# Optimization experiments

Measured on AMD Instinct MI355X. Metric: run time of the kernel, lower is better.

Reference implementation:

```python
import jax, jax.numpy as jnp
import numpy as np

WS = 8      # window_size
NH = 4      # num_heads (fixed in module)

def setup_inputs() -> dict:
    key = jax.random.key(0)
    k1, k2, k3 = jax.random.split(key, 3)
    B, C, H, W = 8, 512, 128, 128
    x = jax.random.normal(k1, (B, C, H, W), dtype=jnp.float32)
    # nn.MultiheadAttention parameters (xavier-ish scale)
    w_in = jax.random.normal(k2, (3 * C, C), dtype=jnp.float32) * (1.0 / np.sqrt(C))
    b_in = jnp.zeros((3 * C,), dtype=jnp.float32)
    w_out = jax.random.normal(k3, (C, C), dtype=jnp.float32) * (1.0 / np.sqrt(C))
    b_out = jnp.zeros((C,), dtype=jnp.float32)
    return {"x": x, "w_in": w_in, "b_in": b_in, "w_out": w_out, "b_out": b_out}

def reference(x, w_in, b_in, w_out, b_out):
    B, C, H, W = x.shape
    Hw, Ww = H // WS, W // WS
    hd = C // NH
    # --- window partition: (B,C,H,W) -> (N, L, C), N = B*Hw*Ww, L = WS*WS ---
    xw = x.reshape(B, C, Hw, WS, Ww, WS)
    xw = xw.transpose(0, 2, 4, 1, 3, 5)            # (B,Hw,Ww,C,WS,WS)
    xw = xw.reshape(-1, C, WS * WS)                # (N, C, L)
    xw = xw.transpose(0, 2, 1)                     # (N, L, C)
    N, L, _ = xw.shape
    # --- fused QKV projection (torch MultiheadAttention in_proj) ---
    qkv = jnp.einsum('nlc,ec->nle', xw, w_in) + b_in   # (N, L, 3C)
    q, k, v = jnp.split(qkv, 3, axis=-1)
    q = q.reshape(N, L, NH, hd)
    k = k.reshape(N, L, NH, hd)
    v = v.reshape(N, L, NH, hd)
    scale = 1.0 / np.sqrt(hd)
    scores = jnp.einsum('nqhd,nkhd->nhqk', q, k) * scale   # (N,NH,L,L)
    attn = jax.nn.softmax(scores, axis=-1)
    ctx = jnp.einsum('nhqk,nkhd->nqhd', attn, v).reshape(N, L, C)
    out = jnp.einsum('nlc,oc->nlo', ctx, w_out) + b_out    # (N, L, C)
    # --- window merge: (N,L,C) -> (B,C,H,W) ---
    out = out.transpose(0, 2, 1)                           # (N, C, L)
    out = out.reshape(B, Hw, Ww, C, WS, WS)
    out = out.transpose(0, 3, 1, 4, 2, 5)                  # (B,C,Hw,WS,Ww,WS)
    return out.reshape(B, C, H, W)
```

## Files before the change

kernel.cpp:

```cpp
#include <hip/hip_runtime.h>


typedef __attribute__((ext_vector_type(8))) short s16x8;
typedef __attribute__((ext_vector_type(4))) float f32x4;

#define C_TOT 512
#define HWIMG 128
#define CH_STRIDE (HWIMG * HWIMG)
#define NWIN 2048
#define XW_ELEMS ((size_t)NWIN * 64 * 512)
#define XW_BYTES (XW_ELEMS * 2ull)
#define WIT_ELEMS 786432ull
#define WOT_ELEMS 262144ull
#define WBF_ELEMS 1048576ull
#define WBF_BYTES (WBF_ELEMS * 2ull)
#define CTX_BYTES_FULL (XW_ELEMS * 2ull)

__device__ __forceinline__ unsigned short f2bf(float f) {
  unsigned u = __float_as_uint(f);
  u += 0x7FFFu + ((u >> 16) & 1u);
  return (unsigned short)(u >> 16);
}

__device__ __forceinline__ void gload_lds16(const void* g, void* l) {
  __builtin_amdgcn_global_load_lds(
      (const __attribute__((address_space(1))) unsigned int*)g,
      (__attribute__((address_space(3))) unsigned int*)l, 16, 0, 0);
}

__global__ void conv_w_kernel(const float* __restrict__ w_in,
                              const float* __restrict__ w_out,
                              unsigned short* __restrict__ wbf) {
  int i = blockIdx.x * blockDim.x + threadIdx.x;
  const int NIN = 3 * C_TOT * C_TOT;
  float v = (i < NIN) ? w_in[i] : w_out[i - NIN];
  wbf[i] = f2bf(v);
}

__global__ void conv_wt_kernel(const float* __restrict__ w_in,
                               const float* __restrict__ w_out,
                               unsigned short* __restrict__ wit,
                               unsigned short* __restrict__ wot) {
  int i = blockIdx.x * blockDim.x + threadIdx.x;
  const int NIN = 3 * C_TOT * C_TOT;
  if (i < NIN) {
    const int e = i >> 9, c = i & 511;
    const int t = e >> 9, rem = e & 511;
    const int h = rem >> 7, d = rem & 127;
    const int m = t * 8 + (d >> 4), l = d & 15;
    const int c8 = c >> 3, ec = c & 7;
    wit[(((size_t)(h * 24 + m) * 64 + c8) << 7) + l * 8 + ec] = f2bf(w_in[i]);
  } else {
    const int j = i - NIN;
    const int od = j >> 9, c = j & 511;
    const int m = od >> 4, l = od & 15;
    const int c8 = c >> 3, ec = c & 7;
    wot[(((size_t)m * 64 + c8) << 7) + l * 8 + ec] = f2bf(w_out[j]);
  }
}

__global__ void __launch_bounds__(256)
pack_x_kernel(const float* __restrict__ x, unsigned short* __restrict__ xw) {
  const int n  = blockIdx.x;
  const int bb = n >> 8, hw = (n >> 4) & 15, ww = n & 15;
  const size_t wbase = (size_t)bb * C_TOT * CH_STRIDE
                     + (size_t)(hw * 8) * HWIMG + (size_t)(ww * 8);
  const int tok = threadIdx.x & 63;
  const int q4  = threadIdx.x >> 6;
  const int r = tok >> 3, cc = tok & 7;
  const float* px = x + wbase + (size_t)r * HWIMG + cc;
  unsigned short* pw = xw + (size_t)n * 32768;
#pragma unroll 4
  for (int j = 0; j < 16; ++j) {
    const int o = q4 * 16 + j;
    float v[8];
#pragma unroll
    for (int k = 0; k < 8; ++k) v[k] = px[(size_t)(8 * o + k) * CH_STRIDE];
    s16x8 pk;
#pragma unroll
    for (int k = 0; k < 8; ++k) pk[k] = (short)f2bf(v[k]);
    *(s16x8*)(pw + ((size_t)o * 64 + tok) * 8) = pk;
  }
}

#define BQO 0
#define BKO 16384
#define BVO 32768
#define BXS 49152
#define BPO 49152
#define BLDS 81920

__global__ void __launch_bounds__(512, 4)
qkv_attn_kernel(const unsigned short* __restrict__ xw,
                const float* __restrict__ bin,
                const unsigned short* __restrict__ wit,
                unsigned short* __restrict__ ctx,
                int n0) {
  __shared__ __align__(16) unsigned char sm[BLDS];

  const int tid  = threadIdx.x;
  const int wv   = tid >> 6;
  const int lane = tid & 63;
  const int l15  = lane & 15;
  const int qd   = lane >> 4;
  const int swA  = (l15 & 7) << 4;

  const int h    = blockIdx.x & 3;
  const int nrel = blockIdx.x >> 2;
  const unsigned short* xww = xw + (size_t)(n0 + nrel) * 32768;

  const float SCALE = 0.08838834764831845f;
  const float L2E   = 1.4426950408889634f;

  f32x4 acc[3][4];
#pragma unroll
  for (int a = 0; a < 3; ++a)
#pragma unroll
    for (int b2 = 0; b2 < 4; ++b2) acc[a][b2] = (f32x4){0.f, 0.f, 0.f, 0.f};

  const unsigned short* arow[3];
  int typ[3], d128s[3];
#pragma unroll
  for (int mi = 0; mi < 3; ++mi) {
    const int d0 = 48 * wv + 16 * mi;
    const int t = d0 >> 7;
    const int d128 = d0 & 127;
    typ[mi] = t; d128s[mi] = d128;
    const int m = t * 8 + (d128 >> 4);
    arow[mi] = wit + ((size_t)(h * 24 + m) << 13) + l15 * 8;
  }

#pragma unroll
  for (int p = 0; p < 2; ++p)
    gload_lds16(xww + p * 4096 + tid * 8, &sm[BXS + p * 8192 + (wv << 10)]);
  __syncthreads();

  for (int s = 0; s < 4; ++s) {
    if (s < 3) {
#pragma unroll
      for (int p = 0; p < 2; ++p)
        gload_lds16(xww + (size_t)(s + 1) * 8192 + p * 4096 + tid * 8,
                    &sm[BXS + ((s + 1) & 1) * 16384 + p * 8192 + (wv << 10)]);
    }
    const int cur = BXS + (s & 1) * 16384;
#pragma unroll
    for (int j = 0; j < 4; ++j) {
      const int c8g = 16 * s + 4 * j + qd;
      const int lb = cur + ((4 * j + qd) << 10);
      s16x8 bx[4];
#pragma unroll
      for (int ni = 0; ni < 4; ++ni)
        bx[ni] = *(const s16x8*)(&sm[lb + (16 * ni + l15) * 16]);
#pragma unroll
      for (int mi = 0; mi < 3; ++mi) {
        const s16x8 af = *(const s16x8*)(arow[mi] + ((size_t)c8g << 7));
#pragma unroll
        for (int ni = 0; ni < 4; ++ni)
          acc[mi][ni] = __builtin_amdgcn_mfma_f32_16x16x32_bf16(af, bx[ni], acc[mi][ni], 0, 0, 0);
      }
    }
    __syncthreads();
  }

#pragma unroll
  for (int mi = 0; mi < 3; ++mi) {
    const int t = typ[mi], d128 = d128s[mi];
    const int e0 = t * 512 + h * 128 + d128 + 4 * qd;
    const float bi0 = bin[e0], bi1 = bin[e0 + 1], bi2 = bin[e0 + 2], bi3 = bin[e0 + 3];
#pragma unroll
    for (int ni = 0; ni < 4; ++ni) {
      const int tok = 16 * ni + l15;
      const unsigned short h0 = f2bf(acc[mi][ni][0] + bi0);
      const unsigned short h1 = f2bf(acc[mi][ni][1] + bi1);
      const unsigned short h2 = f2bf(acc[mi][ni][2] + bi2);
      const unsigned short h3 = f2bf(acc[mi][ni][3] + bi3);
      if (t < 2) {
        const unsigned lo = (unsigned)h0 | ((unsigned)h1 << 16);
        const unsigned hi = (unsigned)h2 | ((unsigned)h3 << 16);
        const unsigned long long pk = (unsigned long long)lo | ((unsigned long long)hi << 32);
        const int base = (t == 0) ? BQO : BKO;
        *(unsigned long long*)(&sm[base + tok * 256 + ((2 * (d128 + 4 * qd)) ^ swA)]) = pk;
      } else {
        const int vd = d128 + 4 * qd;
        *(unsigned short*)(&sm[BVO + (vd    ) * 128 + ((2 * tok) ^ (((vd    ) & 7) << 4))]) = h0;
        *(unsigned short*)(&sm[BVO + (vd + 1) * 128 + ((2 * tok) ^ (((vd + 1) & 7) << 4))]) = h1;
        *(unsigned short*)(&sm[BVO + (vd + 2) * 128 + ((2 * tok) ^ (((vd + 2) & 7) << 4))]) = h2;
        *(unsigned short*)(&sm[BVO + (vd + 3) * 128 + ((2 * tok) ^ (((vd + 3) & 7) << 4))]) = h3;
      }
    }
  }
  __syncthreads();

  if (wv < 4) {
    f32x4 s[4];
#pragma unroll
    for (int a = 0; a < 4; ++a) s[a] = (f32x4){0.f, 0.f, 0.f, 0.f};
    const int tqa = 16 * wv + l15;
#pragma unroll
    for (int ks = 0; ks < 4; ++ks) {
      const int c0 = 32 * ks + 8 * qd;
      const s16x8 aq = *(const s16x8*)(&sm[BQO + tqa * 256 + ((2 * c0) ^ swA)]);
#pragma unroll
      for (int ni = 0; ni < 4; ++ni) {
        const int tk = 16 * ni + l15;
        const s16x8 bk = *(const s16x8*)(&sm[BKO + tk * 256 + ((2 * c0) ^ swA)]);
        s[ni] = __builtin_amdgcn_mfma_f32_16x16x32_bf16(aq, bk, s[ni], 0, 0, 0);
      }
    }
    float sv[4][4];
#pragma unroll
    for (int ni = 0; ni < 4; ++ni)
#pragma unroll
      for (int i = 0; i < 4; ++i) sv[ni][i] = s[ni][i] * SCALE;
    float m[4];
#pragma unroll
    for (int i = 0; i < 4; ++i)
      m[i] = fmaxf(fmaxf(sv[0][i], sv[1][i]), fmaxf(sv[2][i], sv[3][i]));
#pragma unroll
    for (int d = 1; d < 16; d <<= 1)
#pragma unroll
      for (int i = 0; i < 4; ++i) m[i] = fmaxf(m[i], __shfl_xor(m[i], d));
    float p[4][4], sum[4] = {0.f, 0.f, 0.f, 0.f};
#pragma unroll
    for (int ni = 0; ni < 4; ++ni)
#pragma unroll
      for (int i = 0; i < 4; ++i) {
        p[ni][i] = exp2f((sv[ni][i] - m[i]) * L2E);
        sum[i] += p[ni][i];
      }
#pragma unroll
    for (int d = 1; d < 16; d <<= 1)
#pragma unroll
      for (int i = 0; i < 4; ++i) sum[i] += __shfl_xor(sum[i], d);
    float rinv[4];
#pragma unroll
    for (int i = 0; i < 4; ++i) rinv[i] = 1.0f / sum[i];
#pragma unroll
    for (int ni = 0; ni < 4; ++ni)
#pragma unroll
      for (int i = 0; i < 4; ++i) {
        const int tqr = 16 * wv + 4 * qd + i;
        const int tk = 16 * ni + l15;
        *(unsigned short*)(&sm[BPO + tqr * 128 + ((2 * tk) ^ ((tqr & 7) << 4))]) =
            f2bf(p[ni][i] * rinv[i]);
      }
  }
  __syncthreads();

  {
    const int mq = wv >> 1;
    const int nb = (wv & 1) * 4;
    f32x4 cacc[4];
#pragma unroll
    for (int a = 0; a < 4; ++a) cacc[a] = (f32x4){0.f, 0.f, 0.f, 0.f};
    const int tqa = 16 * mq + l15;
#pragma unroll
    for (int ks = 0; ks < 2; ++ks) {
      const int c0 = 32 * ks + 8 * qd;
      const s16x8 ap = *(const s16x8*)(&sm[BPO + tqa * 128 + ((2 * c0) ^ swA)]);
#pragma unroll
      for (int j = 0; j < 4; ++j) {
        const int vda = 16 * (nb + j) + l15;
        const s16x8 bv = *(const s16x8*)(&sm[BVO + vda * 128 + ((2 * c0) ^ swA)]);
        cacc[j] = __builtin_amdgcn_mfma_f32_16x16x32_bf16(ap, bv, cacc[j], 0, 0, 0);
      }
    }
    unsigned short* ctxn = ctx + (size_t)nrel * 32768;
#pragma unroll
    for (int j = 0; j < 4; ++j) {
      const int vd = 16 * (nb + j) + l15;
      const int c  = h * 128 + vd;
      const int c8 = c >> 3, e = c & 7;
#pragma unroll
      for (int i = 0; i < 4; ++i) {
        const int tq = 16 * mq + 4 * qd + i;
        ctxn[((size_t)c8 * 64 + tq) * 8 + e] = f2bf(cacc[j][i]);
      }
    }
  }
}

#define OXS 0
#define OLDS 32768

__global__ void __launch_bounds__(512, 4)
outproj_kernel(const unsigned short* __restrict__ ctx,
               const unsigned short* __restrict__ wot,
               const float* __restrict__ bout,
               float* __restrict__ out, int n0) {
  __shared__ __align__(16) unsigned char sm[OLDS];

  const int tid  = threadIdx.x;
  const int wv   = tid >> 6;
  const int lane = tid & 63;
  const int l15  = lane & 15;
  const int qd   = lane >> 4;

  const int nrel = blockIdx.x;
  const int n  = n0 + nrel;
  const int bb = n >> 8, hw = (n >> 4) & 15, ww = n & 15;
  const size_t wbase = (size_t)bb * C_TOT * CH_STRIDE
                     + (size_t)(hw * 8) * HWIMG + (size_t)(ww * 8);
  const unsigned short* ctxn = ctx + (size_t)nrel * 32768;

  f32x4 oacc[4][4];
#pragma unroll
  for (int a = 0; a < 4; ++a)
#pragma unroll
    for (int b2 = 0; b2 < 4; ++b2) oacc[a][b2] = (f32x4){0.f, 0.f, 0.f, 0.f};

  const unsigned short* orow[4];
#pragma unroll
  for (int mo = 0; mo < 4; ++mo)
    orow[mo] = wot + ((size_t)(4 * wv + mo) << 13) + l15 * 8;

#pragma unroll
  for (int p = 0; p < 2; ++p)
    gload_lds16(ctxn + p * 4096 + tid * 8, &sm[OXS + p * 8192 + (wv << 10)]);
  __syncthreads();

  for (int s = 0; s < 4; ++s) {
    if (s < 3) {
#pragma unroll
      for (int p = 0; p < 2; ++p)
        gload_lds16(ctxn + (size_t)(s + 1) * 8192 + p * 4096 + tid * 8,
                    &sm[OXS + ((s + 1) & 1) * 16384 + p * 8192 + (wv << 10)]);
    }
    const int cur = OXS + (s & 1) * 16384;
#pragma unroll
    for (int j = 0; j < 4; ++j) {
      const int c8g = 16 * s + 4 * j + qd;
      const int lb = cur + ((4 * j + qd) << 10);
      s16x8 bc[4];
#pragma unroll
      for (int ni = 0; ni < 4; ++ni)
        bc[ni] = *(const s16x8*)(&sm[lb + (16 * ni + l15) * 16]);
#pragma unroll
      for (int mo = 0; mo < 4; ++mo) {
        const s16x8 af = *(const s16x8*)(orow[mo] + ((size_t)c8g << 7));
#pragma unroll
        for (int ni = 0; ni < 4; ++ni)
          oacc[mo][ni] = __builtin_amdgcn_mfma_f32_16x16x32_bf16(af, bc[ni], oacc[mo][ni], 0, 0, 0);
      }
    }
    __syncthreads();
  }

#pragma unroll
  for (int mo = 0; mo < 4; ++mo) {
    const int od0 = 64 * wv + 16 * mo + 4 * qd;
    float bo[4];
#pragma unroll
    for (int i = 0; i < 4; ++i) bo[i] = bout[od0 + i];
#pragma unroll
    for (int ni = 0; ni < 4; ++ni) {
      const int tok = 16 * ni + l15;
      const int r = tok >> 3, cc = tok & 7;
#pragma unroll
      for (int i = 0; i < 4; ++i) {
        out[wbase + (size_t)(od0 + i) * CH_STRIDE + (size_t)r * HWIMG + cc] =
            oacc[mo][ni][i] + bo[i];
      }
    }
  }
}

#define QO    0
#define KO    16384
#define VO    32768
#define PO    49152
#define CTXO  57344
#define LDSB  73728

__global__ void __launch_bounds__(512, 2)
local_attn_kernel(const unsigned short* __restrict__ xw,
                  const float* __restrict__ bin,
                  const float* __restrict__ bout,
                  const unsigned short* __restrict__ wi,
                  const unsigned short* __restrict__ wo,
                  float* __restrict__ out) {
  __shared__ __align__(16) unsigned char sm[LDSB];
  const int tid  = threadIdx.x;
  const int wv   = tid >> 6;
  const int lane = tid & 63;
  const int l15  = lane & 15;
  const int qd   = lane >> 4;
  const int swA  = (l15 & 7) << 4;
  const int n  = blockIdx.x;
  const int bb = n >> 8;
  const int hw = (n >> 4) & 15;
  const int ww = n & 15;
  const size_t wbase = (size_t)bb * C_TOT * CH_STRIDE
                     + (size_t)(hw * 8) * HWIMG + (size_t)(ww * 8);
  const unsigned short* xww = xw + (size_t)n * 32768;
  f32x4 oacc[4][4];
#pragma unroll
  for (int a = 0; a < 4; ++a)
#pragma unroll
    for (int b2 = 0; b2 < 4; ++b2) oacc[a][b2] = (f32x4){0.f, 0.f, 0.f, 0.f};
  const float SCALE = 0.08838834764831845f;
  const float L2E   = 1.4426950408889634f;
  for (int h = 0; h < 4; ++h) {
    f32x4 acc[3][4];
#pragma unroll
    for (int a = 0; a < 3; ++a)
#pragma unroll
      for (int b2 = 0; b2 < 4; ++b2) acc[a][b2] = (f32x4){0.f, 0.f, 0.f, 0.f};
    const unsigned short* arow[3];
    int typ[3], d128s[3];
#pragma unroll
    for (int mi = 0; mi < 3; ++mi) {
      const int d0 = 48 * wv + 16 * mi;
      const int t = d0 >> 7;
      const int d128 = d0 & 127;
      typ[mi] = t; d128s[mi] = d128;
      arow[mi] = wi + (size_t)(t * 512 + h * 128 + d128 + l15) * 512;
    }
#pragma unroll 4
    for (int ks = 0; ks < 16; ++ks) {
      const int c0 = 32 * ks + 8 * qd;
      const int c8 = c0 >> 3;
      s16x8 bx[4];
#pragma unroll
      for (int ni = 0; ni < 4; ++ni)
        bx[ni] = *(const s16x8*)(xww + ((size_t)c8 * 64 + 16 * ni + l15) * 8);
#pragma unroll
      for (int mi = 0; mi < 3; ++mi) {
        const s16x8 af = *(const s16x8*)(arow[mi] + c0);
#pragma unroll
        for (int ni = 0; ni < 4; ++ni)
          acc[mi][ni] = __builtin_amdgcn_mfma_f32_16x16x32_bf16(af, bx[ni], acc[mi][ni], 0, 0, 0);
      }
    }
#pragma unroll
    for (int mi = 0; mi < 3; ++mi) {
      const int t = typ[mi], d128 = d128s[mi];
      const int e0 = t * 512 + h * 128 + d128 + 4 * qd;
      const float bi0 = bin[e0], bi1 = bin[e0 + 1], bi2 = bin[e0 + 2], bi3 = bin[e0 + 3];
#pragma unroll
      for (int ni = 0; ni < 4; ++ni) {
        const int tok = 16 * ni + l15;
        const unsigned short h0 = f2bf(acc[mi][ni][0] + bi0);
        const unsigned short h1 = f2bf(acc[mi][ni][1] + bi1);
        const unsigned short h2 = f2bf(acc[mi][ni][2] + bi2);
        const unsigned short h3 = f2bf(acc[mi][ni][3] + bi3);
        if (t < 2) {
          const unsigned lo = (unsigned)h0 | ((unsigned)h1 << 16);
          const unsigned hi = (unsigned)h2 | ((unsigned)h3 << 16);
          const unsigned long long pk = (unsigned long long)lo | ((unsigned long long)hi << 32);
          const int base = (t == 0) ? QO : KO;
          *(unsigned long long*)(&sm[base + tok * 256 + ((2 * (d128 + 4 * qd)) ^ swA)]) = pk;
        } else {
          const int vd = d128 + 4 * qd;
          *(unsigned short*)(&sm[VO + (vd    ) * 128 + ((2 * tok) ^ (((vd    ) & 7) << 4))]) = h0;
          *(unsigned short*)(&sm[VO + (vd + 1) * 128 + ((2 * tok) ^ (((vd + 1) & 7) << 4))]) = h1;
          *(unsigned short*)(&sm[VO + (vd + 2) * 128 + ((2 * tok) ^ (((vd + 2) & 7) << 4))]) = h2;
          *(unsigned short*)(&sm[VO + (vd + 3) * 128 + ((2 * tok) ^ (((vd + 3) & 7) << 4))]) = h3;
        }
      }
    }
    __syncthreads();
    if (wv < 4) {
      f32x4 s[4];
#pragma unroll
      for (int a = 0; a < 4; ++a) s[a] = (f32x4){0.f, 0.f, 0.f, 0.f};
      const int tqa = 16 * wv + l15;
#pragma unroll
      for (int ks = 0; ks < 4; ++ks) {
        const int c0 = 32 * ks + 8 * qd;
        const s16x8 aq = *(const s16x8*)(&sm[QO + tqa * 256 + ((2 * c0) ^ swA)]);
#pragma unroll
        for (int ni = 0; ni < 4; ++ni) {
          const int tk = 16 * ni + l15;
          const s16x8 bk = *(const s16x8*)(&sm[KO + tk * 256 + ((2 * c0) ^ swA)]);
          s[ni] = __builtin_amdgcn_mfma_f32_16x16x32_bf16(aq, bk, s[ni], 0, 0, 0);
        }
      }
      float sv[4][4];
#pragma unroll
      for (int ni = 0; ni < 4; ++ni)
#pragma unroll
        for (int i = 0; i < 4; ++i) sv[ni][i] = s[ni][i] * SCALE;
      float m[4];
#pragma unroll
      for (int i = 0; i < 4; ++i)
        m[i] = fmaxf(fmaxf(sv[0][i], sv[1][i]), fmaxf(sv[2][i], sv[3][i]));
#pragma unroll
      for (int d = 1; d < 16; d <<= 1)
#pragma unroll
        for (int i = 0; i < 4; ++i) m[i] = fmaxf(m[i], __shfl_xor(m[i], d));
      float p[4][4], sum[4] = {0.f, 0.f, 0.f, 0.f};
#pragma unroll
      for (int ni = 0; ni < 4; ++ni)
#pragma unroll
        for (int i = 0; i < 4; ++i) {
          p[ni][i] = exp2f((sv[ni][i] - m[i]) * L2E);
          sum[i] += p[ni][i];
        }
#pragma unroll
      for (int d = 1; d < 16; d <<= 1)
#pragma unroll
        for (int i = 0; i < 4; ++i) sum[i] += __shfl_xor(sum[i], d);
      float rinv[4];
#pragma unroll
      for (int i = 0; i < 4; ++i) rinv[i] = 1.0f / sum[i];
#pragma unroll
      for (int ni = 0; ni < 4; ++ni)
#pragma unroll
        for (int i = 0; i < 4; ++i) {
          const int tqr = 16 * wv + 4 * qd + i;
          const int tk = 16 * ni + l15;
          *(unsigned short*)(&sm[PO + tqr * 128 + ((2 * tk) ^ ((tqr & 7) << 4))]) =
              f2bf(p[ni][i] * rinv[i]);
        }
    }
    __syncthreads();
    {
      const int mq = wv >> 1;
      const int nb = (wv & 1) * 4;
      f32x4 cacc[4];
#pragma unroll
      for (int a = 0; a < 4; ++a) cacc[a] = (f32x4){0.f, 0.f, 0.f, 0.f};
      const int tqa = 16 * mq + l15;
#pragma unroll
      for (int ks = 0; ks < 2; ++ks) {
        const int c0 = 32 * ks + 8 * qd;
        const s16x8 ap = *(const s16x8*)(&sm[PO + tqa * 128 + ((2 * c0) ^ swA)]);
#pragma unroll
        for (int j = 0; j < 4; ++j) {
          const int vda = 16 * (nb + j) + l15;
          const s16x8 bv = *(const s16x8*)(&sm[VO + vda * 128 + ((2 * c0) ^ swA)]);
          cacc[j] = __builtin_amdgcn_mfma_f32_16x16x32_bf16(ap, bv, cacc[j], 0, 0, 0);
        }
      }
#pragma unroll
      for (int j = 0; j < 4; ++j)
#pragma unroll
        for (int i = 0; i < 4; ++i) {
          const int tq = 16 * mq + 4 * qd + i;
          const int vd = 16 * (nb + j) + l15;
          *(unsigned short*)(&sm[CTXO + tq * 256 + ((2 * vd) ^ ((tq & 7) << 4))]) =
              f2bf(cacc[j][i]);
        }
    }
    __syncthreads();
    {
#pragma unroll
      for (int ks = 0; ks < 4; ++ks) {
        const int c0 = 32 * ks + 8 * qd;
        s16x8 a2[4];
#pragma unroll
        for (int mo = 0; mo < 4; ++mo) {
          const int od = 64 * wv + 16 * mo + l15;
          a2[mo] = *(const s16x8*)(&wo[(size_t)od * 512 + 128 * h + c0]);
        }
        s16x8 bc[4];
#pragma unroll
        for (int ni = 0; ni < 4; ++ni) {
          const int tok = 16 * ni + l15;
          bc[ni] = *(const s16x8*)(&sm[CTXO + tok * 256 + ((2 * c0) ^ swA)]);
        }
#pragma unroll
        for (int mo = 0; mo < 4; ++mo)
#pragma unroll
          for (int ni = 0; ni < 4; ++ni)
            oacc[mo][ni] = __builtin_amdgcn_mfma_f32_16x16x32_bf16(a2[mo], bc[ni], oacc[mo][ni], 0, 0, 0);
      }
    }
  }
#pragma unroll
  for (int mo = 0; mo < 4; ++mo) {
    const int od0 = 64 * wv + 16 * mo + 4 * qd;
    float bo[4];
#pragma unroll
    for (int i = 0; i < 4; ++i) bo[i] = bout[od0 + i];
#pragma unroll
    for (int ni = 0; ni < 4; ++ni) {
      const int tok = 16 * ni + l15;
      const int r = tok >> 3, cc = tok & 7;
#pragma unroll
      for (int i = 0; i < 4; ++i) {
        out[wbase + (size_t)(od0 + i) * CH_STRIDE + (size_t)r * HWIMG + cc] =
            oacc[mo][ni][i] + bo[i];
      }
    }
  }
}

extern "C" void kernel_launch(void* const* d_in, const int* in_sizes, int n_in,
                              void* d_out, int out_size, void* d_ws, size_t ws_size,
                              hipStream_t stream) {
  const float* x     = (const float*)d_in[0];
  const float* w_in  = (const float*)d_in[1];
  const float* b_in  = (const float*)d_in[2];
  const float* w_out = (const float*)d_in[3];
  const float* b_out = (const float*)d_in[4];
  float* out = (float*)d_out;

  const size_t TIL_BYTES = (WIT_ELEMS + WOT_ELEMS) * 2ull;
  int nc = 0;
  for (int c = 1; c <= 8; c <<= 1) {
    if (ws_size >= XW_BYTES + TIL_BYTES + CTX_BYTES_FULL / (size_t)c) { nc = c; break; }
  }

  if (nc) {
    unsigned short* xwp = (unsigned short*)d_ws;
    unsigned short* wit = xwp + XW_ELEMS;
    unsigned short* wot = wit + WIT_ELEMS;
    unsigned short* ctx = wot + WOT_ELEMS;
    conv_wt_kernel<<<4096, 256, 0, stream>>>(w_in, w_out, wit, wot);
    pack_x_kernel<<<NWIN, 256, 0, stream>>>(x, xwp);
    const int nwc = NWIN / nc;
    for (int k = 0; k < nc; ++k) {
      qkv_attn_kernel<<<nwc * 4, 512, 0, stream>>>(xwp, b_in, wit, ctx, k * nwc);
      outproj_kernel<<<nwc, 512, 0, stream>>>(ctx, wot, b_out, out, k * nwc);
    }
  } else {
    unsigned short* xwp = (unsigned short*)d_ws;
    unsigned short* wbf = xwp + XW_ELEMS;
    conv_w_kernel<<<4096, 256, 0, stream>>>(w_in, w_out, wbf);
    pack_x_kernel<<<NWIN, 256, 0, stream>>>(x, xwp);
    local_attn_kernel<<<NWIN, 512, 0, stream>>>(xwp, b_in, b_out,
                                                wbf, wbf + 786432, out);
  }
}
```

Before: 672.4 us.

## Coalesce pack_x loads with float4 image rows and regroup attention block order

Rewrites the window-packing kernel so each thread reads four consecutive pixels of an image row as a float4 and emits four packed tokens, replacing strided scalar loads with wide coalesced reads of full 128-pixel rows. The old packing kernel is kept as a fallback for the low-workspace path. It also remaps qkv_attn block indices so that eight consecutive blocks cover eight windows for the same head, which changes L2 locality of head weights versus window inputs. The redundant per-lane conversion code adds instruction overhead but should be removed by the compiler.

```diff
diff --git a/kernel.cpp b/kernel.cpp
--- a/kernel.cpp
+++ b/kernel.cpp
@@ -61,25 +61,48 @@
 
 __global__ void __launch_bounds__(256)
 pack_x_kernel(const float* __restrict__ x, unsigned short* __restrict__ xw) {
-  const int n  = blockIdx.x;
-  const int bb = n >> 8, hw = (n >> 4) & 15, ww = n & 15;
-  const size_t wbase = (size_t)bb * C_TOT * CH_STRIDE
-                     + (size_t)(hw * 8) * HWIMG + (size_t)(ww * 8);
-  const int tok = threadIdx.x & 63;
-  const int q4  = threadIdx.x >> 6;
-  const int r = tok >> 3, cc = tok & 7;
-  const float* px = x + wbase + (size_t)r * HWIMG + cc;
+  const int blk = blockIdx.x;
+  const int bb  = blk >> 8;
+  const int hw  = (blk >> 4) & 15;
+  const int og4 = blk & 15;
+  const int t   = threadIdx.x;
+  const int p0  = 4 * t;
+  const int r   = p0 >> 7;
+  const int col0 = p0 & 127;
+  const int n   = bb * 256 + hw * 16 + (col0 >> 3);
+  const int tok0 = r * 8 + (col0 & 7);
+  const float* xs = x + (size_t)bb * C_TOT * CH_STRIDE
+                  + (size_t)hw * 1024 + p0;
   unsigned short* pw = xw + (size_t)n * 32768;
-#pragma unroll 4
-  for (int j = 0; j < 16; ++j) {
-    const int o = q4 * 16 + j;
-    float v[8];
-#pragma unroll
-    for (int k = 0; k < 8; ++k) v[k] = px[(size_t)(8 * o + k) * CH_STRIDE];
-    s16x8 pk;
-#pragma unroll
-    for (int k = 0; k < 8; ++k) pk[k] = (short)f2bf(v[k]);
-    *(s16x8*)(pw + ((size_t)o * 64 + tok) * 8) = pk;
+#pragma unroll
+  for (int jo = 0; jo < 4; ++jo) {
+    const int o = og4 * 4 + jo;
+    float4 f[8];
+#pragma unroll
+    for (int k = 0; k < 8; ++k)
+      f[k] = *(const float4*)(xs + (size_t)(8 * o + k) * CH_STRIDE);
+#pragma unroll
+    for (int i = 0; i < 4; ++i) {
+      s16x8 pk;
+      pk[0] = (short)f2bf(f[0].x); pk[1] = (short)f2bf(f[1].x);
+      pk[2] = (short)f2bf(f[2].x); pk[3] = (short)f2bf(f[3].x);
+      pk[4] = (short)f2bf(f[4].x); pk[5] = (short)f2bf(f[5].x);
+      pk[6] = (short)f2bf(f[6].x); pk[7] = (short)f2bf(f[7].x);
+      if (i == 0) {
+        pk[0]=(short)f2bf(f[0].x); pk[1]=(short)f2bf(f[1].x); pk[2]=(short)f2bf(f[2].x); pk[3]=(short)f2bf(f[3].x);
+        pk[4]=(short)f2bf(f[4].x); pk[5]=(short)f2bf(f[5].x); pk[6]=(short)f2bf(f[6].x); pk[7]=(short)f2bf(f[7].x);
+      } else if (i == 1) {
+        pk[0]=(short)f2bf(f[0].y); pk[1]=(short)f2bf(f[1].y); pk[2]=(short)f2bf(f[2].y); pk[3]=(short)f2bf(f[3].y);
+        pk[4]=(short)f2bf(f[4].y); pk[5]=(short)f2bf(f[5].y); pk[6]=(short)f2bf(f[6].y); pk[7]=(short)f2bf(f[7].y);
+      } else if (i == 2) {
+        pk[0]=(short)f2bf(f[0].z); pk[1]=(short)f2bf(f[1].z); pk[2]=(short)f2bf(f[2].z); pk[3]=(short)f2bf(f[3].z);
+        pk[4]=(short)f2bf(f[4].z); pk[5]=(short)f2bf(f[5].z); pk[6]=(short)f2bf(f[6].z); pk[7]=(short)f2bf(f[7].z);
+      } else {
+        pk[0]=(short)f2bf(f[0].w); pk[1]=(short)f2bf(f[1].w); pk[2]=(short)f2bf(f[2].w); pk[3]=(short)f2bf(f[3].w);
+        pk[4]=(short)f2bf(f[4].w); pk[5]=(short)f2bf(f[5].w); pk[6]=(short)f2bf(f[6].w); pk[7]=(short)f2bf(f[7].w);
+      }
+      *(s16x8*)(pw + ((size_t)o * 64 + tok0 + i) * 8) = pk;
+    }
   }
 }
 
@@ -105,8 +128,11 @@
   const int qd   = lane >> 4;
   const int swA  = (l15 & 7) << 4;
 
-  const int h    = blockIdx.x & 3;
-  const int nrel = blockIdx.x >> 2;
+  const int blk = blockIdx.x;
+  const int g   = blk & 7;
+  const int q   = blk >> 3;
+  const int h   = q & 3;
+  const int nrel = (q >> 2) * 8 + g;
   const unsigned short* xww = xw + (size_t)(n0 + nrel) * 32768;
 
   const float SCALE = 0.08838834764831845f;
@@ -371,6 +397,30 @@
 #define PO    49152
 #define CTXO  57344
 #define LDSB  73728
+
+__global__ void __launch_bounds__(256)
+pack_x_fb(const float* __restrict__ x, unsigned short* __restrict__ xw) {
+  const int n  = blockIdx.x;
+  const int bb = n >> 8, hw = (n >> 4) & 15, ww = n & 15;
+  const size_t wbase = (size_t)bb * C_TOT * CH_STRIDE
+                     + (size_t)(hw * 8) * HWIMG + (size_t)(ww * 8);
+  const int tok = threadIdx.x & 63;
+  const int q4  = threadIdx.x >> 6;
+  const int r = tok >> 3, cc = tok & 7;
+  const float* px = x + wbase + (size_t)r * HWIMG + cc;
+  unsigned short* pw = xw + (size_t)n * 32768;
+#pragma unroll 4
+  for (int j = 0; j < 16; ++j) {
+    const int o = q4 * 16 + j;
+    float v[8];
+#pragma unroll
+    for (int k = 0; k < 8; ++k) v[k] = px[(size_t)(8 * o + k) * CH_STRIDE];
+    s16x8 pk;
+#pragma unroll
+    for (int k = 0; k < 8; ++k) pk[k] = (short)f2bf(v[k]);
+    *(s16x8*)(pw + ((size_t)o * 64 + tok) * 8) = pk;
+  }
+}
 
 __global__ void __launch_bounds__(512, 2)
 local_attn_kernel(const unsigned short* __restrict__ xw,
@@ -609,7 +659,7 @@
     unsigned short* wot = wit + WIT_ELEMS;
     unsigned short* ctx = wot + WOT_ELEMS;
     conv_wt_kernel<<<4096, 256, 0, stream>>>(w_in, w_out, wit, wot);
-    pack_x_kernel<<<NWIN, 256, 0, stream>>>(x, xwp);
+    pack_x_kernel<<<2048, 256, 0, stream>>>(x, xwp);
     const int nwc = NWIN / nc;
     for (int k = 0; k < nc; ++k) {
       qkv_attn_kernel<<<nwc * 4, 512, 0, stream>>>(xwp, b_in, wit, ctx, k * nwc);
@@ -619,7 +669,7 @@
     unsigned short* xwp = (unsigned short*)d_ws;
     unsigned short* wbf = xwp + XW_ELEMS;
     conv_w_kernel<<<4096, 256, 0, stream>>>(w_in, w_out, wbf);
-    pack_x_kernel<<<NWIN, 256, 0, stream>>>(x, xwp);
+    pack_x_fb<<<NWIN, 256, 0, stream>>>(x, xwp);
     local_attn_kernel<<<NWIN, 512, 0, stream>>>(xwp, b_in, b_out,
                                                 wbf, wbf + 786432, out);
   }
```

After: 591.2 us. -12.1%, faster.
